# Performance work log

Hardware: AMD Instinct MI355X
Metric: run time of the kernel (lower is better)

Reference implementation:

```python
import jax, jax.numpy as jnp
import numpy as np

T, N = 24, 2048
INPUT_DIM, HIDDEN, MEDIATE, SOCIAL, OUT_DIM = 2, 64, 128, 64, 2
N_SIZE = 2
CELL = 0.3
T_OBS, T_PRED = 9, 19
WIN = (N_SIZE + 1) ** 2  # (N_size+1)^2 = 9 window cells


def _social_pool(h, coords, mask):
    """Faithful social pooling for N_size=2, grid_cell_size=0.3.

    torch builds a dynamic grid, scatter-adds every agent's h into its cell,
    then gathers grid[int(x-R):int(x+R), int(y-R):int(y+R)] per agent.
    With R=0.3 and integer positions >= 4 (guaranteed by the margin), that
    slice is exactly the single cell (x-1, y-1), broadcast over the 3x3
    window. We compute it as a pairwise match without materializing a grid.
    Runs under torch.no_grad() -> stop_gradient.
    """
    margin = 2 * N_SIZE * CELL
    lt = jnp.stack([coords[:, 0].min(), coords[:, 1].min()]) - margin
    p = jnp.floor((coords - lt) / CELL).astype(jnp.int32)            # [N,2]
    p = p * mask.astype(jnp.int32)[:, None]                          # masked agents -> cell (0,0)
    q = p - 1                                                        # gathered cell per agent
    match = (p[None, :, 0] == q[:, None, 0]) & (p[None, :, 1] == q[:, None, 1])  # [i,j]
    cell_val = match.astype(h.dtype) @ h                             # [N,hidden] scatter-add + gather
    Hf = jnp.tile(cell_val, (1, WIN)) * mask[:, None]                # broadcast over 3x3 window, flat
    return jax.lax.stop_gradient(Hf)


def _forward(X, part_masks, all_h_t, all_c_t, Y, W_in, b_in, W_soc, b_soc,
             W_ih, W_hh, b_ih, b_hh, W_out, b_out, T_obs, T_pred):
    relu = jax.nn.relu  # dropout_prob = 0 -> Phi == ReLU

    def lstm(z, h, c):
        g = z @ W_ih.T + b_ih + h @ W_hh.T + b_hh
        i, f, gg, o = jnp.split(g, 4, axis=1)
        c = jax.nn.sigmoid(f) * c + jax.nn.sigmoid(i) * jnp.tanh(gg)
        h = jax.nn.sigmoid(o) * jnp.tanh(c)
        return h, c

    def cell_out(r, h, c, coords, m):
        Hf = _social_pool(h, coords, m)
        e = relu(Hf @ W_soc.T + b_soc)
        z = jnp.concatenate([r, e], axis=1)
        h, c = lstm(z, h, c)
        out = (h @ W_out.T + b_out) * m[:, None]
        return h, c, out

    def step_obs(carry, inp):
        h, c = carry
        x, m = inp
        r = relu(x @ W_in.T + b_in)
        h, c, out = cell_out(r, h, c, x, m)
        return (h, c), out

    (h, c), outs_obs = jax.lax.scan(
        step_obs, (all_h_t, all_c_t), (X[:T_obs + 1], part_masks[:T_obs + 1]))

    def step_pred(carry, inp):
        h, c, last_pt, prev_out = carry
        x, m = inp
        r = relu(last_pt @ W_in.T + b_in)
        h, c, out = cell_out(r, h, c, x, m)
        # torch: last_point = outputs[frame_idx - 1] AFTER the frame runs
        return (h, c, prev_out, out), out

    carry0 = (h, c, X[T_obs + 1], outs_obs[-1])
    _, outs_pred = jax.lax.scan(
        step_pred, carry0, (X[T_obs + 1:T_pred + 1], part_masks[T_obs + 1:T_pred + 1]))

    tail = jnp.zeros((X.shape[0] - T_pred - 1, X.shape[1], OUT_DIM), X.dtype)
    return jnp.concatenate([outs_obs, outs_pred, tail], axis=0)


def setup_inputs() -> dict:
    key = jax.random.key(0)
    ks = jax.random.split(key, 13)

    def lin(kw, kb, out_d, in_d):  # torch nn.Linear default init
        lim = 1.0 / float(np.sqrt(in_d))
        W = jax.random.uniform(kw, (out_d, in_d), minval=-lim, maxval=lim, dtype=jnp.float32)
        b = jax.random.uniform(kb, (out_d,), minval=-lim, maxval=lim, dtype=jnp.float32)
        return W, b

    W_in, b_in = lin(ks[0], ks[1], MEDIATE, INPUT_DIM)
    W_soc, b_soc = lin(ks[2], ks[3], SOCIAL, WIN * HIDDEN)
    W_ih, b_ih = lin(ks[4], ks[5], 4 * HIDDEN, MEDIATE + SOCIAL)
    W_hh, b_hh = lin(ks[6], ks[7], 4 * HIDDEN, HIDDEN)
    W_out, b_out = lin(ks[8], ks[9], OUT_DIM, HIDDEN)

    X = jax.random.normal(ks[10], (T, N, INPUT_DIM), dtype=jnp.float32) * 10.0  # meter-scale coords
    part_masks = (jax.random.uniform(ks[11], (T, N)) < 0.9).astype(jnp.float32)  # binary presence mask
    Y = jax.random.normal(ks[12], (T, N, INPUT_DIM), dtype=jnp.float32)  # unused by forward
    all_h_t = jnp.zeros((N, HIDDEN), jnp.float32)
    all_c_t = jnp.zeros((N, HIDDEN), jnp.float32)

    return {"X": X, "part_masks": part_masks, "all_h_t": all_h_t, "all_c_t": all_c_t,
            "Y": Y, "T_obs": T_OBS, "T_pred": T_PRED,
            "W_in": W_in, "b_in": b_in, "W_soc": W_soc, "b_soc": b_soc,
            "W_ih": W_ih, "W_hh": W_hh, "b_ih": b_ih, "b_hh": b_hh,
            "W_out": W_out, "b_out": b_out}


def reference(X, part_masks, all_h_t, all_c_t, Y, T_obs, T_pred,
              W_in, b_in, W_soc, b_soc, W_ih, W_hh, b_ih, b_hh, W_out, b_out):
    return _forward(X, part_masks, all_h_t, all_c_t, Y, W_in, b_in, W_soc, b_soc,
                    W_ih, W_hh, b_ih, b_hh, W_out, b_out, int(T_obs), int(T_pred))
```

## Files before the change

kernel.cpp:

```cpp
#include <hip/hip_runtime.h>
#include <math.h>


#define N_AG   2048
#define STEPS  20
#define CAP    12
#define NSRV   21
#define MAGIC  0x13572468

typedef short short8 __attribute__((ext_vector_type(8)));
typedef float f32x4  __attribute__((ext_vector_type(4)));
union FU { uint4 q; short8 v; };

__device__ __forceinline__ unsigned short bf16rne(float x) {
    unsigned u = __float_as_uint(x);
    unsigned r = (u + 0x7fff + ((u >> 16) & 1)) >> 16;
    return (unsigned short)r;
}

__device__ __forceinline__ int khash(int k) {
    return (int)(((unsigned)k * 2654435761u) >> 21);
}

__device__ __forceinline__ float fsigm(float x) {
    return __builtin_amdgcn_rcpf(1.f + __expf(-x));
}
__device__ __forceinline__ float ftanh(float x) {
    float e = __expf(2.f * x);
    return 1.f - 2.f * __builtin_amdgcn_rcpf(e + 1.f);
}

__device__ __forceinline__ void bar_lds() {
    asm volatile("s_waitcnt lgkmcnt(0)\n\ts_barrier" ::: "memory");
}

__device__ __forceinline__ void ast(int* p_, int v) {
    __hip_atomic_store(p_, v, __ATOMIC_RELAXED, __HIP_MEMORY_SCOPE_AGENT);
}
__device__ __forceinline__ void astf(float* p_, float v) {
    __hip_atomic_store(p_, v, __ATOMIC_RELAXED, __HIP_MEMORY_SCOPE_AGENT);
}
__device__ __forceinline__ unsigned long long aldu64(const unsigned long long* p_) {
    return __hip_atomic_load(p_, __ATOMIC_RELAXED, __HIP_MEMORY_SCOPE_AGENT);
}

struct KP {
    const float *X, *masks, *h_in, *c_in;
    const float *Win, *bin, *Wsoc, *bsoc, *Wih, *Whh, *bih, *bhh, *Wout, *bout;
    float *Wef;
    int *mcnt, *midx, *need, *flags;
    float *out;
    unsigned long long *hist;
};

__global__ __launch_bounds__(512, 1) void k_all(KP p)
{
    __shared__ __align__(16) uint4 zshq[544];
    __shared__ __align__(16) uint4 zslq[544];
    __shared__ float gbuf[16][258];
    __shared__ float cvs[16][64];
    __shared__ float hs[16][68];
    __shared__ float sWefP[64 * 65];
    __shared__ float2 sWinP[16 * 17];
    __shared__ float sBinP[16 * 9];
    __shared__ float sX[11][16][2];
    __shared__ float sMask[STEPS][16];
    __shared__ int   sCnt[STEPS][16];
    __shared__ int   sNeed[19][16];
    __shared__ int   sMidx[STEPS][16][CAP];
    __shared__ float sBsoc[64], sBc[256], sWout[128], sBout[2];
    __shared__ uint4 sE0h[8], sE0l[8];
    __shared__ float olocal[2][16][2];
    __shared__ int kk[N_AG];
    __shared__ int head[N_AG];
    __shared__ int nxt[N_AG];
    __shared__ float red[512];

    const int tid = threadIdx.x;
    const int bxg = blockIdx.x;

    if (bxg < NSRV) {
        const int sb = bxg;
        {
            int lo = sb * 780;
            int hi = (sb == NSRV - 1) ? 16384 : lo + 780;
            for (int i = lo + tid; i < hi; i += 512)
                p.out[20 * N_AG * 2 + i] = 0.f;
        }
        if (sb == 20) {
            for (int i = tid; i < 4096; i += 512) {
                int s = i >> 6, k = i & 63;
                float a = 0.f;
                #pragma unroll
                for (int w = 0; w < 9; w++) a += p.Wsoc[s * 576 + w * 64 + k];
                astf(&p.Wef[i], a);
            }
            __syncthreads();
            if (tid == 0) ast(&p.flags[20], MAGIC);
            return;
        }

        const int t = sb;
        const float* Xt = p.X + t * N_AG * 2;

        float mnx = 1e30f, mny = 1e30f;
        for (int i = tid; i < N_AG; i += 512) {
            mnx = fminf(mnx, Xt[2 * i]);
            mny = fminf(mny, Xt[2 * i + 1]);
        }
        red[tid] = mnx; __syncthreads();
        for (int s = 256; s > 0; s >>= 1) { if (tid < s) red[tid] = fminf(red[tid], red[tid + s]); __syncthreads(); }
        float ltx = red[0]; __syncthreads();
        red[tid] = mny; __syncthreads();
        for (int s = 256; s > 0; s >>= 1) { if (tid < s) red[tid] = fminf(red[tid], red[tid + s]); __syncthreads(); }
        float lty = red[0]; __syncthreads();
        ltx -= 1.2f;
        lty -= 1.2f;

        for (int i = tid; i < N_AG; i += 512) {
            float m = p.masks[t * N_AG + i];
            int px = (int)floorf((Xt[2 * i]     - ltx) / 0.3f);
            int py = (int)floorf((Xt[2 * i + 1] - lty) / 0.3f);
            int im = (int)m;
            px *= im; py *= im;
            kk[i] = px * 65536 + py;
            head[i] = -1;
            if (t >= 1) ast(&p.need[(t - 1) * N_AG + i], 0);
        }
        __syncthreads();
        for (int j = tid; j < N_AG; j += 512) {
            int kj = kk[j];
            if (kj != 0) nxt[j] = atomicExch(&head[khash(kj)], j);
        }
        __syncthreads();
        for (int i = tid; i < N_AG; i += 512) {
            int ki = kk[i];
            int cnt = 0;
            int base = (t * N_AG + i) * CAP;
            if (ki != 0) {
                int tkey = ki - 65537;
                int lst[CAP];
                for (int j = head[khash(tkey)]; j >= 0; j = nxt[j]) {
                    if (kk[j] == tkey) { if (cnt < CAP) lst[cnt] = j; cnt++; }
                }
                if (cnt > CAP) cnt = CAP;
                for (int a = 1; a < cnt; a++) {
                    int v = lst[a]; int b = a - 1;
                    while (b >= 0 && lst[b] > v) { lst[b + 1] = lst[b]; b--; }
                    lst[b + 1] = v;
                }
                for (int a = 0; a < cnt; a++) {
                    ast(&p.midx[base + a], lst[a]);
                    if (t >= 1) ast(&p.need[(t - 1) * N_AG + lst[a]], 1);
                }
            }
            ast(&p.mcnt[t * N_AG + i], cnt);
        }
        __syncthreads();
        if (tid == 0) ast(&p.flags[t], MAGIC);
        return;
    }

    const int bx    = bxg - NSRV;
    const int wbase = bx * 16;
    const int wv    = tid >> 6, lane = tid & 63;
    const int mA    = lane & 15, quad = lane >> 4;
    const int nt0   = 2 * wv;

    if (tid < 256) sBc[tid] = p.bih[tid] + p.bhh[tid];
    if (tid < 128) {
        sWout[tid] = p.Wout[tid];
        int c = tid;
        sWinP[(c >> 3) * 17 + (c & 7)] = make_float2(p.Win[2 * c], p.Win[2 * c + 1]);
        sBinP[(c >> 3) * 9 + (c & 7)] = p.bin[c];
    }
    if (tid < 64) sBsoc[tid] = p.bsoc[tid];
    if (tid < 2)  sBout[tid] = p.bout[tid];
    if (tid < 8) {
        unsigned uh[4], ul[4];
        #pragma unroll
        for (int w = 0; w < 4; w++) {
            float v0 = fmaxf(p.bsoc[tid * 8 + 2 * w], 0.f);
            float v1 = fmaxf(p.bsoc[tid * 8 + 2 * w + 1], 0.f);
            unsigned short h0 = bf16rne(v0), h1 = bf16rne(v1);
            float f0 = __uint_as_float(((unsigned)h0) << 16);
            float f1 = __uint_as_float(((unsigned)h1) << 16);
            unsigned short l0 = bf16rne(v0 - f0), l1 = bf16rne(v1 - f1);
            uh[w] = (unsigned)h0 | ((unsigned)h1 << 16);
            ul[w] = (unsigned)l0 | ((unsigned)l1 << 16);
        }
        sE0h[tid] = make_uint4(uh[0], uh[1], uh[2], uh[3]);
        sE0l[tid] = make_uint4(ul[0], ul[1], ul[2], ul[3]);
    }
    if (tid < 352) { int tt = tid / 32, r = tid % 32;
                     sX[tt][r >> 1][r & 1] = p.X[tt * (N_AG * 2) + (wbase + (r >> 1)) * 2 + (r & 1)]; }
    if (tid < 320) { int tt = tid / 16, m2 = tid % 16;
                     sMask[tt][m2] = p.masks[tt * N_AG + wbase + m2]; }

    float c0, c1;
    {
        int m0 = tid >> 6, h0i = tid & 63, m1 = m0 + 8;
        hs[m0][h0i] = p.h_in[(wbase + m0) * 64 + h0i];
        hs[m1][h0i] = p.h_in[(wbase + m1) * 64 + h0i];
        c0 = p.c_in[(wbase + m0) * 64 + h0i];
        c1 = p.c_in[(wbase + m1) * 64 + h0i];
    }

    FU wh[2][8], wl[2][8];
    #pragma unroll
    for (int e = 0; e < 2; e++) {
        int g = (nt0 + e) * 16 + mA;
        #pragma unroll
        for (int kt = 0; kt < 8; kt++) {
            int k0 = kt * 32 + quad * 8;
            const float* src = (k0 < 192) ? (p.Wih + g * 192 + k0)
                                          : (p.Whh + g * 64 + (k0 - 192));
            unsigned uh[4], ul[4];
            #pragma unroll
            for (int w = 0; w < 4; w++) {
                float a = src[2 * w], b = src[2 * w + 1];
                unsigned short ha = bf16rne(a), hb = bf16rne(b);
                float fa = __uint_as_float(((unsigned)ha) << 16);
                float fb = __uint_as_float(((unsigned)hb) << 16);
                unsigned short la = bf16rne(a - fa), lb = bf16rne(b - fb);
                uh[w] = (unsigned)ha | ((unsigned)hb << 16);
                ul[w] = (unsigned)la | ((unsigned)lb << 16);
            }
            wh[e][kt].q = make_uint4(uh[0], uh[1], uh[2], uh[3]);
            wl[e][kt].q = make_uint4(ul[0], ul[1], ul[2], ul[3]);
        }
    }

    if (tid < NSRV) {
        while (__hip_atomic_load(&p.flags[tid], __ATOMIC_RELAXED,
                                 __HIP_MEMORY_SCOPE_AGENT) != MAGIC) { }
    }
    __syncthreads();

    if (tid < 320) { int tt = tid / 16, m2 = tid % 16;
                     sCnt[tt][m2] = p.mcnt[tt * N_AG + wbase + m2]; }
    if (tid < 304) { int s = tid / 16, m2 = tid % 16;
                     sNeed[s][m2] = p.need[s * N_AG + wbase + m2]; }
    for (int i = tid; i < 4096; i += 512) sWefP[(i >> 6) * 65 + (i & 63)] = p.Wef[i];
    for (int i = tid; i < STEPS * 16 * CAP; i += 512) {
        int tt = i / (16 * CAP), r = i % (16 * CAP), m2 = r / CAP, n = r % CAP;
        sMidx[tt][m2][n] = p.midx[(tt * N_AG + wbase + m2) * CAP + n];
    }
    __syncthreads();

    #pragma unroll 1
    for (int t = 0; t < STEPS; t++) {
        const int m5 = tid >> 5, s5 = tid & 31;
        const int cnt5 = sCnt[t][m5];

        const unsigned long long* hb = p.hist + (size_t)(t - 1) * (N_AG * 64);
        unsigned long long pw0 = 0, pw1 = 0, qw0 = 0, qw1 = 0;
        int rfirst = -1, rsecond = -1;
        if (cnt5 > 0 && t > 0) {
            rfirst = sMidx[t][m5][0];
            pw0 = aldu64(&hb[rfirst * 64 + s5]);
            pw1 = aldu64(&hb[rfirst * 64 + s5 + 32]);
            if (cnt5 > 1) {
                rsecond = sMidx[t][m5][1];
                qw0 = aldu64(&hb[rsecond * 64 + s5]);
                qw1 = aldu64(&hb[rsecond * 64 + s5 + 32]);
            }
        }

        {
            if (s5 < 16) {
                float px, py;
                if (t <= 10) { px = sX[t][m5][0];         py = sX[t][m5][1]; }
                else         { px = olocal[t & 1][m5][0]; py = olocal[t & 1][m5][1]; }
                float v[8];
                #pragma unroll
                for (int j = 0; j < 8; j++) {
                    float2 w2 = sWinP[s5 * 17 + j];
                    v[j] = fmaxf(w2.x * px + w2.y * py + sBinP[s5 * 9 + j], 0.f);
                }
                unsigned uh[4], ul[4];
                #pragma unroll
                for (int w = 0; w < 4; w++) {
                    float v0 = v[2 * w], v1 = v[2 * w + 1];
                    unsigned short h0 = bf16rne(v0), h1 = bf16rne(v1);
                    float f0 = __uint_as_float(((unsigned)h0) << 16);
                    float f1 = __uint_as_float(((unsigned)h1) << 16);
                    unsigned short l0 = bf16rne(v0 - f0), l1 = bf16rne(v1 - f1);
                    uh[w] = (unsigned)h0 | ((unsigned)h1 << 16);
                    ul[w] = (unsigned)l0 | ((unsigned)l1 << 16);
                }
                zshq[s5 * 17 + m5] = make_uint4(uh[0], uh[1], uh[2], uh[3]);
                zslq[s5 * 17 + m5] = make_uint4(ul[0], ul[1], ul[2], ul[3]);
            } else if (s5 < 24) {
                if (cnt5 == 0) {
                    zshq[s5 * 17 + m5] = sE0h[s5 - 16];
                    zslq[s5 * 17 + m5] = sE0l[s5 - 16];
                }
            } else {
                float v[8];
                #pragma unroll
                for (int j = 0; j < 8; j++) v[j] = hs[m5][(s5 - 24) * 8 + j];
                unsigned uh[4], ul[4];
                #pragma unroll
                for (int w = 0; w < 4; w++) {
                    float v0 = v[2 * w], v1 = v[2 * w + 1];
                    unsigned short h0 = bf16rne(v0), h1 = bf16rne(v1);
                    float f0 = __uint_as_float(((unsigned)h0) << 16);
                    float f1 = __uint_as_float(((unsigned)h1) << 16);
                    unsigned short l0 = bf16rne(v0 - f0), l1 = bf16rne(v1 - f1);
                    uh[w] = (unsigned)h0 | ((unsigned)h1 << 16);
                    ul[w] = (unsigned)l0 | ((unsigned)l1 << 16);
                }
                zshq[s5 * 17 + m5] = make_uint4(uh[0], uh[1], uh[2], uh[3]);
                zslq[s5 * 17 + m5] = make_uint4(ul[0], ul[1], ul[2], ul[3]);
            }
        }
        bar_lds();

        f32x4 a0v = {0.f, 0.f, 0.f, 0.f};
        f32x4 a1v = {0.f, 0.f, 0.f, 0.f};
        #pragma unroll
        for (int u = 0; u < 6; u++) {
            const int kt = (u < 4) ? u : u + 2;
            int fi = (kt * 4 + quad) * 17 + mA;
            FU az, bz;
            az.q = zshq[fi];
            bz.q = zslq[fi];
            a0v = __builtin_amdgcn_mfma_f32_16x16x32_bf16(az.v, wh[0][kt].v, a0v, 0, 0, 0);
            a1v = __builtin_amdgcn_mfma_f32_16x16x32_bf16(az.v, wh[1][kt].v, a1v, 0, 0, 0);
            a0v = __builtin_amdgcn_mfma_f32_16x16x32_bf16(bz.v, wh[0][kt].v, a0v, 0, 0, 0);
            a1v = __builtin_amdgcn_mfma_f32_16x16x32_bf16(bz.v, wh[1][kt].v, a1v, 0, 0, 0);
            a0v = __builtin_amdgcn_mfma_f32_16x16x32_bf16(az.v, wl[0][kt].v, a0v, 0, 0, 0);
            a1v = __builtin_amdgcn_mfma_f32_16x16x32_bf16(az.v, wl[1][kt].v, a1v, 0, 0, 0);
        }

        if (cnt5 > 0) {
            float a0 = 0.f, a1 = 0.f;
            if (t == 0) {
                for (int n = 0; n < cnt5; n++) {
                    int r = sMidx[0][m5][n];
                    a0 += p.h_in[r * 64 + s5];
                    a1 += p.h_in[r * 64 + s5 + 32];
                }
            } else {
                const unsigned tagw = (unsigned)t;
                while ((unsigned)(pw0 >> 32) != tagw || (unsigned)(pw1 >> 32) != tagw) {
                    pw0 = aldu64(&hb[rfirst * 64 + s5]);
                    pw1 = aldu64(&hb[rfirst * 64 + s5 + 32]);
                }
                a0 += __uint_as_float((unsigned)pw0);
                a1 += __uint_as_float((unsigned)pw1);
                if (cnt5 > 1) {
                    while ((unsigned)(qw0 >> 32) != tagw || (unsigned)(qw1 >> 32) != tagw) {
                        qw0 = aldu64(&hb[rsecond * 64 + s5]);
                        qw1 = aldu64(&hb[rsecond * 64 + s5 + 32]);
                    }
                    a0 += __uint_as_float((unsigned)qw0);
                    a1 += __uint_as_float((unsigned)qw1);
                    for (int n = 2; n < cnt5; n++) {
                        int r = sMidx[t][m5][n];
                        unsigned long long w0, w1;
                        do {
                            w0 = aldu64(&hb[r * 64 + s5]);
                            w1 = aldu64(&hb[r * 64 + s5 + 32]);
                        } while ((unsigned)(w0 >> 32) != tagw || (unsigned)(w1 >> 32) != tagw);
                        a0 += __uint_as_float((unsigned)w0);
                        a1 += __uint_as_float((unsigned)w1);
                    }
                }
            }
            cvs[m5][s5] = a0; cvs[m5][s5 + 32] = a1;
            float acc0 = sBsoc[s5], acc1 = sBsoc[s5 + 32];
            const float* w0p = &sWefP[s5 * 65];
            const float* w1p = &sWefP[(s5 + 32) * 65];
            for (int k = 0; k < 64; k++) {
                float cv = cvs[m5][k];
                acc0 += cv * w0p[k];
                acc1 += cv * w1p[k];
            }
            acc0 = fmaxf(acc0, 0.f);
            acc1 = fmaxf(acc1, 0.f);
            const int base = (m5 & 1) * 32;
            float v[8];
            #pragma unroll
            for (int jj = 0; jj < 8; jj++) {
                int c = s5 * 8 + jj;
                int srcl = base + ((c < 32 ? c : c - 32) & 31);
                float va = __shfl(acc0, srcl, 64);
                float vb = __shfl(acc1, srcl, 64);
                v[jj] = (c < 32) ? va : vb;
            }
            if (s5 < 8) {
                unsigned uh[4], ul[4];
                #pragma unroll
                for (int w = 0; w < 4; w++) {
                    float v0 = v[2 * w], v1 = v[2 * w + 1];
                    unsigned short h0 = bf16rne(v0), h1 = bf16rne(v1);
                    float f0 = __uint_as_float(((unsigned)h0) << 16);
                    float f1 = __uint_as_float(((unsigned)h1) << 16);
                    unsigned short l0 = bf16rne(v0 - f0), l1 = bf16rne(v1 - f1);
                    uh[w] = (unsigned)h0 | ((unsigned)h1 << 16);
                    ul[w] = (unsigned)l0 | ((unsigned)l1 << 16);
                }
                zshq[(16 + s5) * 17 + m5] = make_uint4(uh[0], uh[1], uh[2], uh[3]);
                zslq[(16 + s5) * 17 + m5] = make_uint4(ul[0], ul[1], ul[2], ul[3]);
            }
        }
        bar_lds();

        #pragma unroll
        for (int kt = 4; kt <= 5; kt++) {
            int fi = (kt * 4 + quad) * 17 + mA;
            FU az, bz;
            az.q = zshq[fi];
            bz.q = zslq[fi];
            a0v = __builtin_amdgcn_mfma_f32_16x16x32_bf16(az.v, wh[0][kt].v, a0v, 0, 0, 0);
            a1v = __builtin_amdgcn_mfma_f32_16x16x32_bf16(az.v, wh[1][kt].v, a1v, 0, 0, 0);
            a0v = __builtin_amdgcn_mfma_f32_16x16x32_bf16(bz.v, wh[0][kt].v, a0v, 0, 0, 0);
            a1v = __builtin_amdgcn_mfma_f32_16x16x32_bf16(bz.v, wh[1][kt].v, a1v, 0, 0, 0);
            a0v = __builtin_amdgcn_mfma_f32_16x16x32_bf16(az.v, wl[0][kt].v, a0v, 0, 0, 0);
            a1v = __builtin_amdgcn_mfma_f32_16x16x32_bf16(az.v, wl[1][kt].v, a1v, 0, 0, 0);
        }
        #pragma unroll
        for (int r = 0; r < 4; r++) {
            int row = quad * 4 + r;
            gbuf[row][nt0 * 16 + mA]       = a0v[r];
            gbuf[row][(nt0 + 1) * 16 + mA] = a1v[r];
        }
        bar_lds();

        {
            int m0 = tid >> 6, hid = tid & 63, m1 = m0 + 8;
            float hn0, hn1;
            {
                float gi = gbuf[m0][hid]       + sBc[hid];
                float gf = gbuf[m0][64 + hid]  + sBc[64 + hid];
                float gR = gbuf[m0][128 + hid] + sBc[128 + hid];
                float go = gbuf[m0][192 + hid] + sBc[192 + hid];
                float cn = fsigm(gf) * c0 + fsigm(gi) * ftanh(gR);
                hn0 = fsigm(go) * ftanh(cn);
                c0 = cn;
                hs[m0][hid] = hn0;
            }
            {
                float gi = gbuf[m1][hid]       + sBc[hid];
                float gf = gbuf[m1][64 + hid]  + sBc[64 + hid];
                float gR = gbuf[m1][128 + hid] + sBc[128 + hid];
                float go = gbuf[m1][192 + hid] + sBc[192 + hid];
                float cn = fsigm(gf) * c1 + fsigm(gi) * ftanh(gR);
                hn1 = fsigm(go) * ftanh(cn);
                c1 = cn;
                hs[m1][hid] = hn1;
            }
            if (t <= 18) {
                unsigned long long* hp = p.hist + (size_t)t * (N_AG * 64);
                unsigned long long tg = ((unsigned long long)(t + 1)) << 32;
                if (sNeed[t][m0])
                    __hip_atomic_store(&hp[(wbase + m0) * 64 + hid],
                                       tg | (unsigned long long)__float_as_uint(hn0),
                                       __ATOMIC_RELAXED, __HIP_MEMORY_SCOPE_AGENT);
                if (sNeed[t][m1])
                    __hip_atomic_store(&hp[(wbase + m1) * 64 + hid],
                                       tg | (unsigned long long)__float_as_uint(hn1),
                                       __ATOMIC_RELAXED, __HIP_MEMORY_SCOPE_AGENT);
            }

            float w0 = sWout[hid], w1 = sWout[64 + hid];
            float p00 = hn0 * w0, p01 = hn0 * w1;
            float p10 = hn1 * w0, p11 = hn1 * w1;
            #pragma unroll
            for (int off = 32; off >= 1; off >>= 1) {
                p00 += __shfl_xor(p00, off);
                p01 += __shfl_xor(p01, off);
                p10 += __shfl_xor(p10, off);
                p11 += __shfl_xor(p11, off);
            }
            if (hid == 0) {
                float mk0 = sMask[t][m0], mk1 = sMask[t][m1];
                float o00 = (p00 + sBout[0]) * mk0, o01 = (p01 + sBout[1]) * mk0;
                float o10 = (p10 + sBout[0]) * mk1, o11 = (p11 + sBout[1]) * mk1;
                p.out[(t * N_AG + wbase + m0) * 2 + 0] = o00;
                p.out[(t * N_AG + wbase + m0) * 2 + 1] = o01;
                p.out[(t * N_AG + wbase + m1) * 2 + 0] = o10;
                p.out[(t * N_AG + wbase + m1) * 2 + 1] = o11;
                olocal[t & 1][m0][0] = o00; olocal[t & 1][m0][1] = o01;
                olocal[t & 1][m1][0] = o10; olocal[t & 1][m1][1] = o11;
            }
        }
        bar_lds();
    }
}

extern "C" void kernel_launch(void* const* d_in, const int* in_sizes, int n_in,
                              void* d_out, int out_size, void* d_ws, size_t ws_size,
                              hipStream_t stream)
{
    KP kp;
    kp.X     = (const float*)d_in[0];
    kp.masks = (const float*)d_in[1];
    kp.h_in  = (const float*)d_in[2];
    kp.c_in  = (const float*)d_in[3];
    kp.Win   = (const float*)d_in[7];
    kp.bin   = (const float*)d_in[8];
    kp.Wsoc  = (const float*)d_in[9];
    kp.bsoc  = (const float*)d_in[10];
    kp.Wih   = (const float*)d_in[11];
    kp.Whh   = (const float*)d_in[12];
    kp.bih   = (const float*)d_in[13];
    kp.bhh   = (const float*)d_in[14];
    kp.Wout  = (const float*)d_in[15];
    kp.bout  = (const float*)d_in[16];
    kp.out   = (float*)d_out;

    unsigned long long* hist = (unsigned long long*)d_ws;
    float* Wef  = (float*)(hist + 19 * N_AG * 64);
    int*   need = (int*)(Wef + 4096);
    int*   mcnt = need + 19 * N_AG;
    int*   midx = mcnt + STEPS * N_AG;
    int*   flags = midx + STEPS * N_AG * CAP;

    kp.hist = hist; kp.Wef = Wef; kp.need = need; kp.mcnt = mcnt;
    kp.midx = midx; kp.flags = flags;

    k_all<<<NSRV + 128, 512, 0, stream>>>(kp);
}
```

Before: 184.9 us.

## Fuse next-step input packing into LSTM epilogue to drop a per-step barrier

Moves the per-step packing of the input embedding, hidden state and default social features into the tail of the previous step's LSTM update. Each wave now packs its own two agents, keeping outputs in registers instead of shared memory. This removes one block barrier and one LDS phase per time step, plus the olocal buffer. The trade is that 48 lanes per wave do the packing serially after the shuffle reduction, which may lengthen that phase. A pack8 helper also replaces the repeated inline split-bf16 code.

```diff
diff --git a/kernel.cpp b/kernel.cpp
--- a/kernel.cpp
+++ b/kernel.cpp
@@ -16,6 +16,22 @@
     unsigned u = __float_as_uint(x);
     unsigned r = (u + 0x7fff + ((u >> 16) & 1)) >> 16;
     return (unsigned short)r;
+}
+
+__device__ __forceinline__ void pack8(const float* v, uint4& hq, uint4& lq) {
+    unsigned uh[4], ul[4];
+    #pragma unroll
+    for (int w = 0; w < 4; w++) {
+        float v0 = v[2 * w], v1 = v[2 * w + 1];
+        unsigned short h0 = bf16rne(v0), h1 = bf16rne(v1);
+        float f0 = __uint_as_float(((unsigned)h0) << 16);
+        float f1 = __uint_as_float(((unsigned)h1) << 16);
+        unsigned short l0 = bf16rne(v0 - f0), l1 = bf16rne(v1 - f1);
+        uh[w] = (unsigned)h0 | ((unsigned)h1 << 16);
+        ul[w] = (unsigned)l0 | ((unsigned)l1 << 16);
+    }
+    hq = make_uint4(uh[0], uh[1], uh[2], uh[3]);
+    lq = make_uint4(ul[0], ul[1], ul[2], ul[3]);
 }
 
 __device__ __forceinline__ int khash(int k) {
@@ -70,7 +86,6 @@
     __shared__ int   sMidx[STEPS][16][CAP];
     __shared__ float sBsoc[64], sBc[256], sWout[128], sBout[2];
     __shared__ uint4 sE0h[8], sE0l[8];
-    __shared__ float olocal[2][16][2];
     __shared__ int kk[N_AG];
     __shared__ int head[N_AG];
     __shared__ int nxt[N_AG];
@@ -166,6 +181,7 @@
     const int wv    = tid >> 6, lane = tid & 63;
     const int mA    = lane & 15, quad = lane >> 4;
     const int nt0   = 2 * wv;
+    const int m0w   = wv, m1w = wv + 8;
 
     if (tid < 256) sBc[tid] = p.bih[tid] + p.bhh[tid];
     if (tid < 128) {
@@ -177,20 +193,10 @@
     if (tid < 64) sBsoc[tid] = p.bsoc[tid];
     if (tid < 2)  sBout[tid] = p.bout[tid];
     if (tid < 8) {
-        unsigned uh[4], ul[4];
+        float v[8];
         #pragma unroll
-        for (int w = 0; w < 4; w++) {
-            float v0 = fmaxf(p.bsoc[tid * 8 + 2 * w], 0.f);
-            float v1 = fmaxf(p.bsoc[tid * 8 + 2 * w + 1], 0.f);
-            unsigned short h0 = bf16rne(v0), h1 = bf16rne(v1);
-            float f0 = __uint_as_float(((unsigned)h0) << 16);
-            float f1 = __uint_as_float(((unsigned)h1) << 16);
-            unsigned short l0 = bf16rne(v0 - f0), l1 = bf16rne(v1 - f1);
-            uh[w] = (unsigned)h0 | ((unsigned)h1 << 16);
-            ul[w] = (unsigned)l0 | ((unsigned)l1 << 16);
-        }
-        sE0h[tid] = make_uint4(uh[0], uh[1], uh[2], uh[3]);
-        sE0l[tid] = make_uint4(ul[0], ul[1], ul[2], ul[3]);
+        for (int j = 0; j < 8; j++) v[j] = fmaxf(p.bsoc[tid * 8 + j], 0.f);
+        pack8(v, sE0h[tid], sE0l[tid]);
     }
     if (tid < 352) { int tt = tid / 32, r = tid % 32;
                      sX[tt][r >> 1][r & 1] = p.X[tt * (N_AG * 2) + (wbase + (r >> 1)) * 2 + (r & 1)]; }
@@ -199,11 +205,10 @@
 
     float c0, c1;
     {
-        int m0 = tid >> 6, h0i = tid & 63, m1 = m0 + 8;
-        hs[m0][h0i] = p.h_in[(wbase + m0) * 64 + h0i];
-        hs[m1][h0i] = p.h_in[(wbase + m1) * 64 + h0i];
-        c0 = p.c_in[(wbase + m0) * 64 + h0i];
-        c1 = p.c_in[(wbase + m1) * 64 + h0i];
+        hs[m0w][lane] = p.h_in[(wbase + m0w) * 64 + lane];
+        hs[m1w][lane] = p.h_in[(wbase + m1w) * 64 + lane];
+        c0 = p.c_in[(wbase + m0w) * 64 + lane];
+        c1 = p.c_in[(wbase + m1w) * 64 + lane];
     }
 
     FU wh[2][8], wl[2][8];
@@ -215,19 +220,10 @@
             int k0 = kt * 32 + quad * 8;
             const float* src = (k0 < 192) ? (p.Wih + g * 192 + k0)
                                           : (p.Whh + g * 64 + (k0 - 192));
-            unsigned uh[4], ul[4];
+            float v[8];
             #pragma unroll
-            for (int w = 0; w < 4; w++) {
-                float a = src[2 * w], b = src[2 * w + 1];
-                unsigned short ha = bf16rne(a), hb = bf16rne(b);
-                float fa = __uint_as_float(((unsigned)ha) << 16);
-                float fb = __uint_as_float(((unsigned)hb) << 16);
-                unsigned short la = bf16rne(a - fa), lb = bf16rne(b - fb);
-                uh[w] = (unsigned)ha | ((unsigned)hb << 16);
-                ul[w] = (unsigned)la | ((unsigned)lb << 16);
-            }
-            wh[e][kt].q = make_uint4(uh[0], uh[1], uh[2], uh[3]);
-            wl[e][kt].q = make_uint4(ul[0], ul[1], ul[2], ul[3]);
+            for (int j = 0; j < 8; j++) v[j] = src[j];
+            pack8(v, wh[e][kt].q, wl[e][kt].q);
         }
     }
 
@@ -247,6 +243,38 @@
         sMidx[tt][m2][n] = p.midx[(tt * N_AG + wbase + m2) * CAP + n];
     }
     __syncthreads();
+
+    {
+        if (lane < 32) {
+            int a = lane & 1, s5r = lane >> 1;
+            int m = a ? m1w : m0w;
+            float px = sX[0][m][0], py = sX[0][m][1];
+            float v[8];
+            #pragma unroll
+            for (int j = 0; j < 8; j++) {
+                float2 w2 = sWinP[s5r * 17 + j];
+                v[j] = fmaxf(w2.x * px + w2.y * py + sBinP[s5r * 9 + j], 0.f);
+            }
+            pack8(v, zshq[s5r * 17 + m], zslq[s5r * 17 + m]);
+        } else if (lane < 48) {
+            int idx = lane - 32, a = idx & 1, s58 = idx >> 1;
+            int m = a ? m1w : m0w;
+            float v[8];
+            #pragma unroll
+            for (int j = 0; j < 8; j++) v[j] = hs[m][s58 * 8 + j];
+            pack8(v, zshq[(24 + s58) * 17 + m], zslq[(24 + s58) * 17 + m]);
+        } else {
+            int idx = lane - 48, a = idx & 1, s58 = idx >> 1;
+            int m = a ? m1w : m0w;
+            if (sCnt[0][m] == 0) {
+                zshq[(16 + s58) * 17 + m] = sE0h[s58];
+                zslq[(16 + s58) * 17 + m] = sE0l[s58];
+            }
+        }
+    }
+    bar_lds();
+
+    float op0x = 0.f, op0y = 0.f, op1x = 0.f, op1y = 0.f;
 
     #pragma unroll 1
     for (int t = 0; t < STEPS; t++) {
@@ -266,56 +294,6 @@
                 qw1 = aldu64(&hb[rsecond * 64 + s5 + 32]);
             }
         }
-
-        {
-            if (s5 < 16) {
-                float px, py;
-                if (t <= 10) { px = sX[t][m5][0];         py = sX[t][m5][1]; }
-                else         { px = olocal[t & 1][m5][0]; py = olocal[t & 1][m5][1]; }
-                float v[8];
-                #pragma unroll
-                for (int j = 0; j < 8; j++) {
-                    float2 w2 = sWinP[s5 * 17 + j];
-                    v[j] = fmaxf(w2.x * px + w2.y * py + sBinP[s5 * 9 + j], 0.f);
-                }
-                unsigned uh[4], ul[4];
-                #pragma unroll
-                for (int w = 0; w < 4; w++) {
-                    float v0 = v[2 * w], v1 = v[2 * w + 1];
-                    unsigned short h0 = bf16rne(v0), h1 = bf16rne(v1);
-                    float f0 = __uint_as_float(((unsigned)h0) << 16);
-                    float f1 = __uint_as_float(((unsigned)h1) << 16);
-                    unsigned short l0 = bf16rne(v0 - f0), l1 = bf16rne(v1 - f1);
-                    uh[w] = (unsigned)h0 | ((unsigned)h1 << 16);
-                    ul[w] = (unsigned)l0 | ((unsigned)l1 << 16);
-                }
-                zshq[s5 * 17 + m5] = make_uint4(uh[0], uh[1], uh[2], uh[3]);
-                zslq[s5 * 17 + m5] = make_uint4(ul[0], ul[1], ul[2], ul[3]);
-            } else if (s5 < 24) {
-                if (cnt5 == 0) {
-                    zshq[s5 * 17 + m5] = sE0h[s5 - 16];
-                    zslq[s5 * 17 + m5] = sE0l[s5 - 16];
-                }
-            } else {
-                float v[8];
-                #pragma unroll
-                for (int j = 0; j < 8; j++) v[j] = hs[m5][(s5 - 24) * 8 + j];
-                unsigned uh[4], ul[4];
-                #pragma unroll
-                for (int w = 0; w < 4; w++) {
-                    float v0 = v[2 * w], v1 = v[2 * w + 1];
-                    unsigned short h0 = bf16rne(v0), h1 = bf16rne(v1);
-                    float f0 = __uint_as_float(((unsigned)h0) << 16);
-                    float f1 = __uint_as_float(((unsigned)h1) << 16);
-                    unsigned short l0 = bf16rne(v0 - f0), l1 = bf16rne(v1 - f1);
-                    uh[w] = (unsigned)h0 | ((unsigned)h1 << 16);
-                    ul[w] = (unsigned)l0 | ((unsigned)l1 << 16);
-                }
-                zshq[s5 * 17 + m5] = make_uint4(uh[0], uh[1], uh[2], uh[3]);
-                zslq[s5 * 17 + m5] = make_uint4(ul[0], ul[1], ul[2], ul[3]);
-            }
-        }
-        bar_lds();
 
         f32x4 a0v = {0.f, 0.f, 0.f, 0.f};
         f32x4 a1v = {0.f, 0.f, 0.f, 0.f};
@@ -390,21 +368,8 @@
                 float vb = __shfl(acc1, srcl, 64);
                 v[jj] = (c < 32) ? va : vb;
             }
-            if (s5 < 8) {
-                unsigned uh[4], ul[4];
-                #pragma unroll
-                for (int w = 0; w < 4; w++) {
-                    float v0 = v[2 * w], v1 = v[2 * w + 1];
-                    unsigned short h0 = bf16rne(v0), h1 = bf16rne(v1);
-                    float f0 = __uint_as_float(((unsigned)h0) << 16);
-                    float f1 = __uint_as_float(((unsigned)h1) << 16);
-                    unsigned short l0 = bf16rne(v0 - f0), l1 = bf16rne(v1 - f1);
-                    uh[w] = (unsigned)h0 | ((unsigned)h1 << 16);
-                    ul[w] = (unsigned)l0 | ((unsigned)l1 << 16);
-                }
-                zshq[(16 + s5) * 17 + m5] = make_uint4(uh[0], uh[1], uh[2], uh[3]);
-                zslq[(16 + s5) * 17 + m5] = make_uint4(ul[0], ul[1], ul[2], ul[3]);
-            }
+            if (s5 < 8)
+                pack8(v, zshq[(16 + s5) * 17 + m5], zslq[(16 + s5) * 17 + m5]);
         }
         bar_lds();
 
@@ -430,37 +395,37 @@
         bar_lds();
 
         {
-            int m0 = tid >> 6, hid = tid & 63, m1 = m0 + 8;
+            const int hid = lane;
             float hn0, hn1;
             {
-                float gi = gbuf[m0][hid]       + sBc[hid];
-                float gf = gbuf[m0][64 + hid]  + sBc[64 + hid];
-                float gR = gbuf[m0][128 + hid] + sBc[128 + hid];
-                float go = gbuf[m0][192 + hid] + sBc[192 + hid];
+                float gi = gbuf[m0w][hid]       + sBc[hid];
+                float gf = gbuf[m0w][64 + hid]  + sBc[64 + hid];
+                float gR = gbuf[m0w][128 + hid] + sBc[128 + hid];
+                float go = gbuf[m0w][192 + hid] + sBc[192 + hid];
                 float cn = fsigm(gf) * c0 + fsigm(gi) * ftanh(gR);
                 hn0 = fsigm(go) * ftanh(cn);
                 c0 = cn;
-                hs[m0][hid] = hn0;
+                hs[m0w][hid] = hn0;
             }
             {
-                float gi = gbuf[m1][hid]       + sBc[hid];
-                float gf = gbuf[m1][64 + hid]  + sBc[64 + hid];
-                float gR = gbuf[m1][128 + hid] + sBc[128 + hid];
-                float go = gbuf[m1][192 + hid] + sBc[192 + hid];
+                float gi = gbuf[m1w][hid]       + sBc[hid];
+                float gf = gbuf[m1w][64 + hid]  + sBc[64 + hid];
+                float gR = gbuf[m1w][128 + hid] + sBc[128 + hid];
+                float go = gbuf[m1w][192 + hid] + sBc[192 + hid];
                 float cn = fsigm(gf) * c1 + fsigm(gi) * ftanh(gR);
                 hn1 = fsigm(go) * ftanh(cn);
                 c1 = cn;
-                hs[m1][hid] = hn1;
+                hs[m1w][hid] = hn1;
             }
             if (t <= 18) {
                 unsigned long long* hp = p.hist + (size_t)t * (N_AG * 64);
                 unsigned long long tg = ((unsigned long long)(t + 1)) << 32;
-                if (sNeed[t][m0])
-                    __hip_atomic_store(&hp[(wbase + m0) * 64 + hid],
+                if (sNeed[t][m0w])
+                    __hip_atomic_store(&hp[(wbase + m0w) * 64 + hid],
                                        tg | (unsigned long long)__float_as_uint(hn0),
                                        __ATOMIC_RELAXED, __HIP_MEMORY_SCOPE_AGENT);
-                if (sNeed[t][m1])
-                    __hip_atomic_store(&hp[(wbase + m1) * 64 + hid],
+                if (sNeed[t][m1w])
+                    __hip_atomic_store(&hp[(wbase + m1w) * 64 + hid],
                                        tg | (unsigned long long)__float_as_uint(hn1),
                                        __ATOMIC_RELAXED, __HIP_MEMORY_SCOPE_AGENT);
             }
@@ -475,17 +440,48 @@
                 p10 += __shfl_xor(p10, off);
                 p11 += __shfl_xor(p11, off);
             }
-            if (hid == 0) {
-                float mk0 = sMask[t][m0], mk1 = sMask[t][m1];
-                float o00 = (p00 + sBout[0]) * mk0, o01 = (p01 + sBout[1]) * mk0;
-                float o10 = (p10 + sBout[0]) * mk1, o11 = (p11 + sBout[1]) * mk1;
-                p.out[(t * N_AG + wbase + m0) * 2 + 0] = o00;
-                p.out[(t * N_AG + wbase + m0) * 2 + 1] = o01;
-                p.out[(t * N_AG + wbase + m1) * 2 + 0] = o10;
-                p.out[(t * N_AG + wbase + m1) * 2 + 1] = o11;
-                olocal[t & 1][m0][0] = o00; olocal[t & 1][m0][1] = o01;
-                olocal[t & 1][m1][0] = o10; olocal[t & 1][m1][1] = o11;
-            }
+            float mk0 = sMask[t][m0w], mk1 = sMask[t][m1w];
+            float o00 = (p00 + sBout[0]) * mk0, o01 = (p01 + sBout[1]) * mk0;
+            float o10 = (p10 + sBout[0]) * mk1, o11 = (p11 + sBout[1]) * mk1;
+            if (lane == 0)
+                *(float2*)&p.out[(t * N_AG + wbase + m0w) * 2] = make_float2(o00, o01);
+            if (lane == 1)
+                *(float2*)&p.out[(t * N_AG + wbase + m1w) * 2] = make_float2(o10, o11);
+
+            if (t < STEPS - 1) {
+                const int tn = t + 1;
+                if (lane < 32) {
+                    int a = lane & 1, s5r = lane >> 1;
+                    int m = a ? m1w : m0w;
+                    float px, py;
+                    if (tn <= 10) { px = sX[tn][m][0]; py = sX[tn][m][1]; }
+                    else          { px = a ? op1x : op0x;
+                                    py = a ? op1y : op0y; }
+                    float v[8];
+                    #pragma unroll
+                    for (int j = 0; j < 8; j++) {
+                        float2 w2 = sWinP[s5r * 17 + j];
+                        v[j] = fmaxf(w2.x * px + w2.y * py + sBinP[s5r * 9 + j], 0.f);
+                    }
+                    pack8(v, zshq[s5r * 17 + m], zslq[s5r * 17 + m]);
+                } else if (lane < 48) {
+                    int idx = lane - 32, a = idx & 1, s58 = idx >> 1;
+                    int m = a ? m1w : m0w;
+                    float v[8];
+                    #pragma unroll
+                    for (int j = 0; j < 8; j++) v[j] = hs[m][s58 * 8 + j];
+                    pack8(v, zshq[(24 + s58) * 17 + m], zslq[(24 + s58) * 17 + m]);
+                } else {
+                    int idx = lane - 48, a = idx & 1, s58 = idx >> 1;
+                    int m = a ? m1w : m0w;
+                    if (sCnt[tn][m] == 0) {
+                        zshq[(16 + s58) * 17 + m] = sE0h[s58];
+                        zslq[(16 + s58) * 17 + m] = sE0l[s58];
+                    }
+                }
+            }
+            op0x = o00; op0y = o01;
+            op1x = o10; op1y = o11;
         }
         bar_lds();
     }
```

New measurement: 184.6 us. Within noise of the previous version (-0.1%).
